# Kernel optimization log

Hardware: AMD Instinct MI355X
Metric: run time of the kernel (lower is better)

Reference implementation:

```python
import jax, jax.numpy as jnp
import numpy as np

M1 = 16
M2 = 16

def _spectral_conv(x, w1c, w2c):
    # x: [B,C,H,W] real; w*c: [C,C,M1,M2] complex
    B, C, H, W = x.shape
    xft = jnp.fft.rfft2(x)                      # [B,C,H,W//2+1]
    top = jnp.einsum('bixy,ioxy->boxy', xft[:, :, :M1, :M2], w1c)
    bot = jnp.einsum('bixy,ioxy->boxy', xft[:, :, -M1:, :M2], w2c)
    out_ft = jnp.zeros((B, w1c.shape[1], H, W // 2 + 1), dtype=xft.dtype)
    out_ft = out_ft.at[:, :, :M1, :M2].set(top)
    out_ft = out_ft.at[:, :, -M1:, :M2].set(bot)
    return jnp.fft.irfft2(out_ft, s=(H, W))

def _fourier_layer(x, w1c, w2c, cw, cb):
    x1 = _spectral_conv(x, w1c, w2c)
    x2 = jnp.einsum('bchw,oc->bohw', x, cw) + cb[None, :, None, None]  # 1x1 conv
    return jax.nn.gelu(x1 + x2, approximate=False)

def setup_inputs() -> dict:
    key = jax.random.key(0)
    ks = jax.random.split(key, 12)
    B, H, W, Tin, C, step = 8, 256, 256, 10, 32, 5
    scale = 1.0 / (C * C)
    return {
        'x': jax.random.normal(ks[0], (B, H, W, Tin), dtype=jnp.float32),
        'fc0_w': jax.random.normal(ks[1], (Tin + 2, C), dtype=jnp.float32) * 0.1,
        'fc0_b': jax.random.normal(ks[2], (C,), dtype=jnp.float32) * 0.1,
        'w1': jax.random.uniform(ks[3], (6, C, C, M1, M2, 2), dtype=jnp.float32) * scale,
        'w2': jax.random.uniform(ks[4], (6, C, C, M1, M2, 2), dtype=jnp.float32) * scale,
        'conv_w': jax.random.normal(ks[5], (6, C, C), dtype=jnp.float32) * 0.1,
        'conv_b': jax.random.normal(ks[6], (6, C), dtype=jnp.float32) * 0.1,
        'fc1_w': jax.random.normal(ks[7], (C, 128), dtype=jnp.float32) * 0.1,
        'fc1_b': jax.random.normal(ks[8], (128,), dtype=jnp.float32) * 0.1,
        'fc2_w': jax.random.normal(ks[9], (128, step), dtype=jnp.float32) * 0.1,
        'fc2_b': jax.random.normal(ks[10], (step,), dtype=jnp.float32) * 0.1,
    }

def reference(x, fc0_w, fc0_b, w1, w2, conv_w, conv_b, fc1_w, fc1_b, fc2_w, fc2_b):
    B, H, W, _ = x.shape
    gridx = jnp.broadcast_to(jnp.linspace(0.0, 1.0, H, dtype=x.dtype)[None, :, None, None], (B, H, W, 1))
    gridy = jnp.broadcast_to(jnp.linspace(0.0, 1.0, W, dtype=x.dtype)[None, None, :, None], (B, H, W, 1))
    h = jnp.concatenate([x, gridx, gridy], axis=-1)          # [B,H,W,T_in+2]
    h = jnp.einsum('bhwc,cd->bhwd', h, fc0_w) + fc0_b        # lift
    h = jnp.transpose(h, (0, 3, 1, 2))                        # [B,C,H,W]
    w1c = jax.lax.complex(w1[..., 0], w1[..., 1])
    w2c = jax.lax.complex(w2[..., 0], w2[..., 1])
    f = lambda z, i: _fourier_layer(z, w1c[i], w2c[i], conv_w[i], conv_b[i])
    h0 = f(h, 0)
    h = f(h, 1)
    h = f(h, 2) + h0
    h1 = f(h, 3)
    h = f(h, 4)
    h = f(h, 5) + h1
    h = jnp.transpose(h, (0, 2, 3, 1))                        # [B,H,W,C]
    h = jax.nn.gelu(jnp.einsum('bhwc,cd->bhwd', h, fc1_w) + fc1_b, approximate=False)
    return jnp.einsum('bhwc,cd->bhwd', h, fc2_w) + fc2_b      # [B,H,W,step]
```

## Files before the change

### kernel.cpp

```cpp
#include <hip/hip_runtime.h>
#include <math.h>

#define C_ 32
#define H_ 256
#define W_ 256
#define HW_ 65536
#define CHW_ 2097152
#define TWO_PI 6.28318530717958647692f

typedef __bf16 bf16x8 __attribute__((ext_vector_type(8)));
typedef float  f32x4  __attribute__((ext_vector_type(4)));

__device__ __forceinline__ bf16x8 as_bf16x8(uint4 u) {
    return __builtin_bit_cast(bf16x8, u);
}
__device__ __forceinline__ unsigned short bfbits(__bf16 h) {
    return __builtin_bit_cast(unsigned short, h);
}
__device__ __forceinline__ bf16x8 mk8(unsigned a, unsigned b, unsigned c, unsigned d) {
    return __builtin_bit_cast(bf16x8, make_uint4(a, b, c, d));
}
__device__ __forceinline__ unsigned rot16(unsigned v) { return (v >> 16) | (v << 16); }
__device__ __forceinline__ uint2 splitpack(float x, float y) {
    __bf16 xh = (__bf16)x, yh = (__bf16)y;
    float xl = x - (float)xh, yl = y - (float)yh;
    unsigned hi = (unsigned)bfbits(xh) | ((unsigned)bfbits(yh) << 16);
    unsigned lo = (unsigned)bfbits((__bf16)xl) | ((unsigned)bfbits((__bf16)yl) << 16);
    return make_uint2(hi, lo);
}

__device__ __forceinline__ float gelu_exact(float x) {
    return 0.5f * x * (1.0f + erff(x * 0.7071067811865475f));
}

__device__ __forceinline__ void build_tw(float2* tw, int tid) {
    float a = TWO_PI * (1.0f / 256.0f) * (float)tid;
    float s_, c_; sincosf(a, &s_, &c_);
    tw[tid] = make_float2(c_, s_);
}
__device__ __forceinline__ void build_twbf(uint2* twbf, int tid) {
    float a = TWO_PI * (1.0f / 256.0f) * (float)tid;
    float s_, c_; sincosf(a, &s_, &c_);
    twbf[tid] = splitpack(c_, s_);
}

__global__ void k_probe(float* __restrict__ out, float ws_kib) {
    if (threadIdx.x == 0 && blockIdx.x == 0) out[0] = ws_kib;
}

__global__ __launch_bounds__(256)
void k_lift(const float* __restrict__ xb, const float* __restrict__ fc0_w,
            const float* __restrict__ fc0_b, float* __restrict__ out) {
    __shared__ float wsh[12 * 32];
    __shared__ float bsh[32];
    int tid = threadIdx.x;
    for (int n = tid; n < 384; n += 256) wsh[n] = fc0_w[n];
    if (tid < 32) bsh[tid] = fc0_b[tid];
    __syncthreads();
    int p = blockIdx.x * 256 + tid;
    int w = p & 255;
    int h = (p >> 8) & 255;
    float in[12];
    const float* xp = xb + (size_t)p * 10;
    #pragma unroll
    for (int t = 0; t < 10; ++t) in[t] = xp[t];
    in[10] = (float)h * (1.0f / 255.0f);
    in[11] = (float)w * (1.0f / 255.0f);
    float* op = out + (p & 0xFFFF) + (size_t)(p >> 16) * CHW_;
    #pragma unroll
    for (int c = 0; c < 32; ++c) {
        float acc = bsh[c];
        #pragma unroll
        for (int t = 0; t < 12; ++t) acc += in[t] * wsh[t * 32 + c];
        op[(size_t)c * HW_] = acc;
    }
}

__global__ __launch_bounds__(256)
void k_dftw_mfma(const float* __restrict__ X, float* __restrict__ S, int nTiles) {
    __shared__ __align__(16) unsigned short twf[16384];
    int tid = threadIdx.x;
    for (int f = tid; f < 8192; f += 256) {
        int i  = f & 7;
        int c  = (f >> 3) & 15;
        int g  = (f >> 7) & 3;
        int nt = (f >> 9) & 1;
        int kk = f >> 10;
        int k  = kk * 32 + 8 * g + i;
        int j  = nt * 16 + c;
        int kx = j >> 1;
        int a  = (k * kx) & 255;
        float ang = (float)a * (TWO_PI / 256.0f);
        float s_, c_; sincosf(ang, &s_, &c_);
        float val = (j & 1) ? -s_ : c_;
        __bf16 hi = (__bf16)val;
        float  r  = val - (float)hi;
        __bf16 lo = (__bf16)r;
        twf[f]        = bfbits(hi);
        twf[8192 + f] = bfbits(lo);
    }
    __syncthreads();
    int wv   = tid >> 6;
    int lane = tid & 63;
    int kg   = lane >> 4;
    int cl   = lane & 15;
    const uint4* twp = (const uint4*)twf;
    for (int tile = blockIdx.x * 4 + wv; tile < nTiles; tile += gridDim.x * 4) {
        const float* xr = X + (size_t)(tile * 16 + cl) * 256 + 8 * kg;
        f32x4 acc0 = {0.f, 0.f, 0.f, 0.f};
        f32x4 acc1 = {0.f, 0.f, 0.f, 0.f};
        #pragma unroll
        for (int kk = 0; kk < 8; ++kk) {
            float4 a0 = *(const float4*)(xr + kk * 32);
            float4 a1 = *(const float4*)(xr + kk * 32 + 4);
            float xv[8] = {a0.x, a0.y, a0.z, a0.w, a1.x, a1.y, a1.z, a1.w};
            bf16x8 Ah, Al;
            #pragma unroll
            for (int i = 0; i < 8; ++i) {
                __bf16 h = (__bf16)xv[i];
                Ah[i] = h;
                Al[i] = (__bf16)(xv[i] - (float)h);
            }
            int base = kk * 128 + kg * 16 + cl;
            bf16x8 Bh0 = as_bf16x8(twp[base]);
            bf16x8 Bh1 = as_bf16x8(twp[base + 64]);
            bf16x8 Bl0 = as_bf16x8(twp[base + 1024]);
            bf16x8 Bl1 = as_bf16x8(twp[base + 1088]);
            acc0 = __builtin_amdgcn_mfma_f32_16x16x32_bf16(Al, Bl0, acc0, 0, 0, 0);
            acc0 = __builtin_amdgcn_mfma_f32_16x16x32_bf16(Ah, Bl0, acc0, 0, 0, 0);
            acc0 = __builtin_amdgcn_mfma_f32_16x16x32_bf16(Al, Bh0, acc0, 0, 0, 0);
            acc0 = __builtin_amdgcn_mfma_f32_16x16x32_bf16(Ah, Bh0, acc0, 0, 0, 0);
            acc1 = __builtin_amdgcn_mfma_f32_16x16x32_bf16(Al, Bl1, acc1, 0, 0, 0);
            acc1 = __builtin_amdgcn_mfma_f32_16x16x32_bf16(Ah, Bl1, acc1, 0, 0, 0);
            acc1 = __builtin_amdgcn_mfma_f32_16x16x32_bf16(Al, Bh1, acc1, 0, 0, 0);
            acc1 = __builtin_amdgcn_mfma_f32_16x16x32_bf16(Ah, Bh1, acc1, 0, 0, 0);
        }
        float* sp = S + (size_t)(tile * 16 + 4 * kg) * 32 + cl;
        #pragma unroll
        for (int q = 0; q < 4; ++q) {
            sp[q * 32]      = acc0[q];
            sp[q * 32 + 16] = acc1[q];
        }
    }
}

__global__ __launch_bounds__(256)
void k_dfth(const float* __restrict__ S, float* __restrict__ G) {
    __shared__ uint2 twbf[256];
    __shared__ uint2 slp[256][17];
    int tid = threadIdx.x;
    build_twbf(twbf, tid);
    const float2* sp = (const float2*)S + (size_t)blockIdx.x * 4096;
    #pragma unroll
    for (int i = 0; i < 16; ++i) {
        int n = i * 256 + tid;
        float2 v = sp[n];
        slp[n >> 4][n & 15] = splitpack(v.x, v.y);
    }
    __syncthreads();
    int wv = tid >> 6, lane = tid & 63, kg = lane >> 4, cl = lane & 15;
    int mt = wv >> 1, nt = wv & 1;
    int kyi_row = mt * 16 + cl;
    int ky = (kyi_row < 16) ? kyi_row : (kyi_row + 224);
    f32x4 acc = {0.f, 0.f, 0.f, 0.f};
    #pragma unroll 4
    for (int kk = 0; kk < 16; ++kk) {
        unsigned Ah[4], Al[4], Bh[4], Bl[4];
        #pragma unroll
        for (int j2 = 0; j2 < 4; ++j2) {
            int h = kk * 16 + kg * 4 + j2;
            uint2 t = twbf[(ky * h) & 255];
            Ah[j2] = t.x; Al[j2] = t.y;
            uint2 d = slp[h][cl];
            if (nt == 0) { Bh[j2] = d.x;                       Bl[j2] = d.y; }
            else         { Bh[j2] = rot16(d.x) ^ 0x80000000u;  Bl[j2] = rot16(d.y) ^ 0x80000000u; }
        }
        bf16x8 ah = mk8(Ah[0], Ah[1], Ah[2], Ah[3]);
        bf16x8 al = mk8(Al[0], Al[1], Al[2], Al[3]);
        bf16x8 bh = mk8(Bh[0], Bh[1], Bh[2], Bh[3]);
        bf16x8 bl = mk8(Bl[0], Bl[1], Bl[2], Bl[3]);
        acc = __builtin_amdgcn_mfma_f32_16x16x32_bf16(al, bl, acc, 0, 0, 0);
        acc = __builtin_amdgcn_mfma_f32_16x16x32_bf16(ah, bl, acc, 0, 0, 0);
        acc = __builtin_amdgcn_mfma_f32_16x16x32_bf16(al, bh, acc, 0, 0, 0);
        acc = __builtin_amdgcn_mfma_f32_16x16x32_bf16(ah, bh, acc, 0, 0, 0);
    }
    float* gf = G + (((size_t)blockIdx.x * 512 + (size_t)(mt * 16 + 4 * kg) * 16 + cl) * 2 + nt);
    #pragma unroll
    for (int q = 0; q < 4; ++q) gf[q * 32] = acc[q];
}

__global__ __launch_bounds__(256)
void k_mix(const float* __restrict__ G, const float* __restrict__ w1,
           const float* __restrict__ w2, float* __restrict__ G2) {
    int t = blockIdx.x * 256 + threadIdx.x;
    int kx  = t & 15;
    int kyi = (t >> 4) & 31;
    int o   = (t >> 9) & 31;
    int b   = t >> 14;
    const float* wp = (kyi < 16) ? w1 : w2;
    int kyj = kyi & 15;
    const float2* gp = (const float2*)G + (size_t)b * 16384 + (size_t)kyi * 16 + kx;
    float ar = 0.f, ai = 0.f;
    for (int i = 0; i < 32; ++i) {
        float2 g = gp[(size_t)i * 512];
        const float* wv = wp + ((((size_t)(i * 32 + o)) * 16 + kyj) * 16 + kx) * 2;
        ar += g.x * wv[0] - g.y * wv[1];
        ai += g.x * wv[1] + g.y * wv[0];
    }
    ((float2*)G2)[t] = make_float2(ar, ai);
}

__global__ __launch_bounds__(256)
void k_idfth(const float* __restrict__ G2, float* __restrict__ T) {
    __shared__ uint2 twbf[256];
    __shared__ uint2 gre[32][17];
    __shared__ uint2 gim[32][17];
    int tid = threadIdx.x;
    build_twbf(twbf, tid);
    const float2* gp = (const float2*)G2 + (size_t)blockIdx.x * 512;
    for (int n = tid; n < 512; n += 256) {
        float2 v = gp[n];
        gre[n >> 4][n & 15] = splitpack(v.x, -v.y);
        gim[n >> 4][n & 15] = splitpack(v.y,  v.x);
    }
    __syncthreads();
    int wv = tid >> 6, lane = tid & 63, kg = lane >> 4, cl = lane & 15;
    f32x4 accR[4] = {{0,0,0,0},{0,0,0,0},{0,0,0,0},{0,0,0,0}};
    f32x4 accI[4] = {{0,0,0,0},{0,0,0,0},{0,0,0,0},{0,0,0,0}};
    #pragma unroll
    for (int kk = 0; kk < 2; ++kk) {
        unsigned Brh[4], Brl[4], Bih[4], Bil[4];
        #pragma unroll
        for (int j2 = 0; j2 < 4; ++j2) {
            int kyi = kk * 16 + 4 * kg + j2;
            uint2 dr = gre[kyi][cl]; Brh[j2] = dr.x; Brl[j2] = dr.y;
            uint2 di = gim[kyi][cl]; Bih[j2] = di.x; Bil[j2] = di.y;
        }
        bf16x8 brh = mk8(Brh[0], Brh[1], Brh[2], Brh[3]);
        bf16x8 brl = mk8(Brl[0], Brl[1], Brl[2], Brl[3]);
        bf16x8 bih = mk8(Bih[0], Bih[1], Bih[2], Bih[3]);
        bf16x8 bil = mk8(Bil[0], Bil[1], Bil[2], Bil[3]);
        #pragma unroll
        for (int m = 0; m < 4; ++m) {
            int h = (wv * 4 + m) * 16 + cl;
            unsigned Ah[4], Al[4];
            #pragma unroll
            for (int j2 = 0; j2 < 4; ++j2) {
                int kyi = kk * 16 + 4 * kg + j2;
                int ky  = (kk == 0) ? kyi : (kyi + 224);
                uint2 t = twbf[(ky * h) & 255];
                Ah[j2] = t.x; Al[j2] = t.y;
            }
            bf16x8 ah = mk8(Ah[0], Ah[1], Ah[2], Ah[3]);
            bf16x8 al = mk8(Al[0], Al[1], Al[2], Al[3]);
            accR[m] = __builtin_amdgcn_mfma_f32_16x16x32_bf16(al, brl, accR[m], 0, 0, 0);
            accR[m] = __builtin_amdgcn_mfma_f32_16x16x32_bf16(ah, brl, accR[m], 0, 0, 0);
            accR[m] = __builtin_amdgcn_mfma_f32_16x16x32_bf16(al, brh, accR[m], 0, 0, 0);
            accR[m] = __builtin_amdgcn_mfma_f32_16x16x32_bf16(ah, brh, accR[m], 0, 0, 0);
            accI[m] = __builtin_amdgcn_mfma_f32_16x16x32_bf16(al, bil, accI[m], 0, 0, 0);
            accI[m] = __builtin_amdgcn_mfma_f32_16x16x32_bf16(ah, bil, accI[m], 0, 0, 0);
            accI[m] = __builtin_amdgcn_mfma_f32_16x16x32_bf16(al, bih, accI[m], 0, 0, 0);
            accI[m] = __builtin_amdgcn_mfma_f32_16x16x32_bf16(ah, bih, accI[m], 0, 0, 0);
        }
    }
    float sc = (cl == 0 ? 1.0f : 2.0f) * (1.0f / 65536.0f);
    float2* tp = (float2*)T;
    #pragma unroll
    for (int m = 0; m < 4; ++m) {
        #pragma unroll
        for (int q = 0; q < 4; ++q) {
            int h = (wv * 4 + m) * 16 + 4 * kg + q;
            tp[((size_t)blockIdx.x * 256 + h) * 16 + cl] =
                make_float2(accR[m][q] * sc, accI[m][q] * sc);
        }
    }
}

__global__ __launch_bounds__(256)
void k_invw_conv(const float* __restrict__ T, const float* X,
                 const float* __restrict__ cw, const float* __restrict__ cb,
                 const float* __restrict__ skip, float* Y) {
    __shared__ float2 tw[256];
    __shared__ float2 tsh[32][17];
    int tid = threadIdx.x;
    build_tw(tw, tid);
    int b  = blockIdx.x >> 8;
    int hh = blockIdx.x & 255;
    const float2* tp = (const float2*)T;
    for (int n = tid; n < 512; n += 256) {
        int o = n >> 4, kx = n & 15;
        tsh[o][kx] = tp[(((size_t)(b * 32 + o)) * 256 + hh) * 16 + kx];
    }
    __syncthreads();
    int wv = tid >> 6, lane = tid & 63;
    int kg = lane >> 4, cl = lane & 15;

    bf16x8 Ash[2], Asl[2];
    bf16x8 Ach[2], Acl2[2];
    #pragma unroll
    for (int mt = 0; mt < 2; ++mt) {
        int o = mt * 16 + cl;
        const float4* cwp = (const float4*)(cw + o * 32 + 8 * kg);
        float4 c0 = cwp[0], c1 = cwp[1];
        float cvv[8] = {c0.x, c0.y, c0.z, c0.w, c1.x, c1.y, c1.z, c1.w};
        #pragma unroll
        for (int j = 0; j < 8; ++j) {
            int k = 8 * kg + j;
            float2 tv = tsh[o][k >> 1];
            float v = (k & 1) ? -tv.y : tv.x;
            __bf16 hv = (__bf16)v;
            Ash[mt][j] = hv;
            Asl[mt][j] = (__bf16)(v - (float)hv);
            float cv = cvv[j];
            __bf16 hc = (__bf16)cv;
            Ach[mt][j]  = hc;
            Acl2[mt][j] = (__bf16)(cv - (float)hc);
        }
    }

    f32x4 acc[2][4];
    #pragma unroll
    for (int mt = 0; mt < 2; ++mt)
        #pragma unroll
        for (int nt = 0; nt < 4; ++nt)
            #pragma unroll
            for (int q = 0; q < 4; ++q)
                acc[mt][nt][q] = cb[mt * 16 + 4 * kg + q];

    const float* xb = X + (size_t)b * CHW_ + (size_t)hh * W_;
    #pragma unroll
    for (int nt = 0; nt < 4; ++nt) {
        int w = 64 * wv + 16 * nt + cl;
        bf16x8 Bth, Btl, Bxh, Bxl;
        #pragma unroll
        for (int j = 0; j < 8; ++j) {
            int k = 8 * kg + j;
            float2 cs = tw[((k >> 1) * w) & 255];
            float v = (k & 1) ? cs.y : cs.x;
            __bf16 hv = (__bf16)v;
            Bth[j] = hv;
            Btl[j] = (__bf16)(v - (float)hv);
            float xv = xb[(size_t)k * HW_ + w];
            __bf16 hx = (__bf16)xv;
            Bxh[j] = hx;
            Bxl[j] = (__bf16)(xv - (float)hx);
        }
        #pragma unroll
        for (int mt = 0; mt < 2; ++mt) {
            acc[mt][nt] = __builtin_amdgcn_mfma_f32_16x16x32_bf16(Asl[mt],  Btl, acc[mt][nt], 0, 0, 0);
            acc[mt][nt] = __builtin_amdgcn_mfma_f32_16x16x32_bf16(Ash[mt],  Btl, acc[mt][nt], 0, 0, 0);
            acc[mt][nt] = __builtin_amdgcn_mfma_f32_16x16x32_bf16(Asl[mt],  Bth, acc[mt][nt], 0, 0, 0);
            acc[mt][nt] = __builtin_amdgcn_mfma_f32_16x16x32_bf16(Ash[mt],  Bth, acc[mt][nt], 0, 0, 0);
            acc[mt][nt] = __builtin_amdgcn_mfma_f32_16x16x32_bf16(Acl2[mt], Bxl, acc[mt][nt], 0, 0, 0);
            acc[mt][nt] = __builtin_amdgcn_mfma_f32_16x16x32_bf16(Ach[mt],  Bxl, acc[mt][nt], 0, 0, 0);
            acc[mt][nt] = __builtin_amdgcn_mfma_f32_16x16x32_bf16(Acl2[mt], Bxh, acc[mt][nt], 0, 0, 0);
            acc[mt][nt] = __builtin_amdgcn_mfma_f32_16x16x32_bf16(Ach[mt],  Bxh, acc[mt][nt], 0, 0, 0);
        }
    }

    const bool hasSkip = (skip != nullptr);
    #pragma unroll
    for (int mt = 0; mt < 2; ++mt) {
        #pragma unroll
        for (int q = 0; q < 4; ++q) {
            int o = 16 * mt + 4 * kg + q;
            size_t rowbase = (size_t)b * CHW_ + (size_t)o * HW_ + (size_t)hh * W_;
            #pragma unroll
            for (int nt = 0; nt < 4; ++nt) {
                int w = 64 * wv + 16 * nt + cl;
                float g = gelu_exact(acc[mt][nt][q]);
                if (hasSkip) g += skip[rowbase + w];
                Y[rowbase + w] = g;
            }
        }
    }
}

__global__ __launch_bounds__(256)
void k_mlp(const float* __restrict__ X, const float* __restrict__ fc1_w,
           const float* __restrict__ fc1_b, const float* __restrict__ fc2_w,
           const float* __restrict__ fc2_b, float* __restrict__ outb) {
    int tid = threadIdx.x;
    int p0 = blockIdx.x * 512 + tid;
    int b  = p0 >> 16;
    int hw = p0 & 0xFFFF;
    const float* xp = X + (size_t)b * CHW_ + hw;
    float xv0[32], xv1[32];
    #pragma unroll
    for (int i = 0; i < 32; ++i) {
        xv0[i] = xp[(size_t)i * HW_];
        xv1[i] = xp[(size_t)i * HW_ + 256];
    }
    float o50[5] = {0.f, 0.f, 0.f, 0.f, 0.f};
    float o51[5] = {0.f, 0.f, 0.f, 0.f, 0.f};
    #pragma unroll 4
    for (int d = 0; d < 128; ++d) {
        float bd = fc1_b[d];
        float a0 = bd, a1 = bd;
        #pragma unroll
        for (int i = 0; i < 32; ++i) {
            float wv = fc1_w[i * 128 + d];
            a0 += xv0[i] * wv;
            a1 += xv1[i] * wv;
        }
        float g0 = gelu_exact(a0);
        float g1 = gelu_exact(a1);
        #pragma unroll
        for (int s = 0; s < 5; ++s) {
            float w2v = fc2_w[d * 5 + s];
            o50[s] += g0 * w2v;
            o51[s] += g1 * w2v;
        }
    }
    float* op0 = outb + (size_t)p0 * 5;
    #pragma unroll
    for (int s = 0; s < 5; ++s) op0[s] = o50[s] + fc2_b[s];
    float* op1 = outb + ((size_t)p0 + 256) * 5;
    #pragma unroll
    for (int s = 0; s < 5; ++s) op1[s] = o51[s] + fc2_b[s];
}

extern "C" void kernel_launch(void* const* d_in, const int* in_sizes, int n_in,
                              void* d_out, int out_size, void* d_ws, size_t ws_size,
                              hipStream_t stream) {
    const float* x      = (const float*)d_in[0];
    const float* fc0_w  = (const float*)d_in[1];
    const float* fc0_b  = (const float*)d_in[2];
    const float* w1     = (const float*)d_in[3];
    const float* w2     = (const float*)d_in[4];
    const float* conv_w = (const float*)d_in[5];
    const float* conv_b = (const float*)d_in[6];
    const float* fc1_w  = (const float*)d_in[7];
    const float* fc1_b  = (const float*)d_in[8];
    const float* fc2_w  = (const float*)d_in[9];
    const float* fc2_b  = (const float*)d_in[10];
    float* out = (float*)d_out;

    const size_t ACTb = 16777216;
    const size_t ACTi = 2097152;
    const size_t STb = 2097152, Gb = 262144;
    const size_t STi = 262144,  Gi = 32768;

    if (ws_size >= 2 * ACTb * sizeof(float)) {
        float* A0 = (float*)d_ws;
        float* A1 = A0 + ACTb;
        float* ST = out;
        float* G  = ST + STb;
        float* G2 = G + Gb;

        k_lift<<<2048, 256, 0, stream>>>(x, fc0_w, fc0_b, A0);
        auto layer = [&](int l, const float* Xin, float* Yout, const float* skip) {
            k_dftw_mfma<<<512, 256, 0, stream>>>(Xin, ST, 4096);
            k_dfth<<<256, 256, 0, stream>>>(ST, G);
            k_mix<<<512, 256, 0, stream>>>(G, w1 + (size_t)l * 524288,
                                           w2 + (size_t)l * 524288, G2);
            k_idfth<<<256, 256, 0, stream>>>(G2, ST);
            k_invw_conv<<<2048, 256, 0, stream>>>(ST, Xin, conv_w + (size_t)l * 1024,
                                                  conv_b + (size_t)l * 32, skip, Yout);
        };
        layer(0, A0, A1, nullptr);
        layer(1, A0, A0, nullptr);
        layer(2, A0, A0, A1);
        layer(3, A0, A1, nullptr);
        layer(4, A0, A0, nullptr);
        layer(5, A0, A0, A1);
        k_mlp<<<1024, 256, 0, stream>>>(A0, fc1_w, fc1_b, fc2_w, fc2_b, out);

    } else if (ws_size >= (3 * ACTi + STi + 2 * Gi) * sizeof(float)) {
        float* A0 = (float*)d_ws;
        float* A1 = A0 + ACTi;
        float* A2 = A1 + ACTi;
        float* ST = A2 + ACTi;
        float* G  = ST + STi;
        float* G2 = G + Gi;

        auto layer = [&](int l, const float* Xin, float* Yout, const float* skip) {
            k_dftw_mfma<<<64, 256, 0, stream>>>(Xin, ST, 512);
            k_dfth<<<32, 256, 0, stream>>>(ST, G);
            k_mix<<<64, 256, 0, stream>>>(G, w1 + (size_t)l * 524288,
                                          w2 + (size_t)l * 524288, G2);
            k_idfth<<<32, 256, 0, stream>>>(G2, ST);
            k_invw_conv<<<256, 256, 0, stream>>>(ST, Xin, conv_w + (size_t)l * 1024,
                                                 conv_b + (size_t)l * 32, skip, Yout);
        };
        for (int b = 0; b < 8; ++b) {
            k_lift<<<256, 256, 0, stream>>>(x + (size_t)b * HW_ * 10, fc0_w, fc0_b, A0);
            layer(0, A0, A2, nullptr);
            layer(1, A0, A1, nullptr);
            layer(2, A1, A0, A2);
            layer(3, A0, A2, nullptr);
            layer(4, A0, A1, nullptr);
            layer(5, A1, A0, A2);
            k_mlp<<<128, 256, 0, stream>>>(A0, fc1_w, fc1_b, fc2_w, fc2_b,
                                           out + (size_t)b * 327680);
        }
    } else {
        k_probe<<<1, 64, 0, stream>>>(out, (float)(ws_size >> 10));
    }
}
```

Before: 649.8 us.

## Run MLP head fc1 on MFMA with split-bf16 precision and shared-memory staging

Rewrites the final per-pixel MLP kernel so the 32x128 fc1 matmul runs on bf16 MFMA. Both operands are split into hi and lo bf16 parts and combined with four MFMAs to keep near-fp32 accuracy. Weights are packed into shared memory, the gelu outputs go to an LDS tile, and fc2 is done as a reduction across four lanes with shuffles. The grid becomes a grid-stride loop over 64-pixel chunks. The aim is to replace scalar FMA work and repeated global weight loads, at the cost of extra syncs and LDS traffic.

```diff
diff --git a/kernel.cpp b/kernel.cpp
--- a/kernel.cpp
+++ b/kernel.cpp
@@ -379,45 +379,80 @@
 __global__ __launch_bounds__(256)
 void k_mlp(const float* __restrict__ X, const float* __restrict__ fc1_w,
            const float* __restrict__ fc1_b, const float* __restrict__ fc2_w,
-           const float* __restrict__ fc2_b, float* __restrict__ outb) {
+           const float* __restrict__ fc2_b, float* __restrict__ outb, int nChunks) {
+    __shared__ uint2 w1p[2048];
+    __shared__ float bsh[128];
+    __shared__ float w2sh[640];
+    __shared__ float Gsh[64][133];
     int tid = threadIdx.x;
-    int p0 = blockIdx.x * 512 + tid;
-    int b  = p0 >> 16;
-    int hw = p0 & 0xFFFF;
-    const float* xp = X + (size_t)b * CHW_ + hw;
-    float xv0[32], xv1[32];
-    #pragma unroll
-    for (int i = 0; i < 32; ++i) {
-        xv0[i] = xp[(size_t)i * HW_];
-        xv1[i] = xp[(size_t)i * HW_ + 256];
-    }
-    float o50[5] = {0.f, 0.f, 0.f, 0.f, 0.f};
-    float o51[5] = {0.f, 0.f, 0.f, 0.f, 0.f};
-    #pragma unroll 4
-    for (int d = 0; d < 128; ++d) {
-        float bd = fc1_b[d];
-        float a0 = bd, a1 = bd;
-        #pragma unroll
-        for (int i = 0; i < 32; ++i) {
-            float wv = fc1_w[i * 128 + d];
-            a0 += xv0[i] * wv;
-            a1 += xv1[i] * wv;
-        }
-        float g0 = gelu_exact(a0);
-        float g1 = gelu_exact(a1);
-        #pragma unroll
-        for (int s = 0; s < 5; ++s) {
-            float w2v = fc2_w[d * 5 + s];
-            o50[s] += g0 * w2v;
-            o51[s] += g1 * w2v;
-        }
-    }
-    float* op0 = outb + (size_t)p0 * 5;
-    #pragma unroll
-    for (int s = 0; s < 5; ++s) op0[s] = o50[s] + fc2_b[s];
-    float* op1 = outb + ((size_t)p0 + 256) * 5;
-    #pragma unroll
-    for (int s = 0; s < 5; ++s) op1[s] = o51[s] + fc2_b[s];
+    for (int f = tid; f < 2048; f += 256) {
+        int j2 = f & 3, cl = (f >> 2) & 15, kg = (f >> 6) & 3, nt = f >> 8;
+        int d = nt * 16 + cl, k0 = 8 * kg + 2 * j2;
+        w1p[f] = splitpack(fc1_w[k0 * 128 + d], fc1_w[(k0 + 1) * 128 + d]);
+    }
+    if (tid < 128) bsh[tid] = fc1_b[tid];
+    for (int f = tid; f < 640; f += 256) w2sh[f] = fc2_w[f];
+    float b2[5];
+    #pragma unroll
+    for (int s = 0; s < 5; ++s) b2[s] = fc2_b[s];
+    int wv = tid >> 6, lane = tid & 63, kg = lane >> 4, cl = lane & 15;
+    int ploc2 = tid >> 2, dq = tid & 3;
+    __syncthreads();
+    for (int chunk = blockIdx.x; chunk < nChunks; chunk += gridDim.x) {
+        int P0 = chunk * 64;
+        int b  = P0 >> 16;
+        int hw0 = P0 & 0xFFFF;
+        {
+            const float* xp = X + (size_t)b * CHW_ + (size_t)(8 * kg) * HW_
+                            + (hw0 + wv * 16 + cl);
+            bf16x8 Ah, Al;
+            #pragma unroll
+            for (int j = 0; j < 8; ++j) {
+                float v = xp[(size_t)j * HW_];
+                __bf16 h = (__bf16)v;
+                Ah[j] = h;
+                Al[j] = (__bf16)(v - (float)h);
+            }
+            #pragma unroll
+            for (int nt = 0; nt < 8; ++nt) {
+                const uint2* wp = &w1p[((nt * 4 + kg) * 16 + cl) * 4];
+                uint2 q0 = wp[0], q1 = wp[1], q2 = wp[2], q3 = wp[3];
+                bf16x8 Bh = mk8(q0.x, q1.x, q2.x, q3.x);
+                bf16x8 Bl = mk8(q0.y, q1.y, q2.y, q3.y);
+                float bv = bsh[nt * 16 + cl];
+                f32x4 acc = {bv, bv, bv, bv};
+                acc = __builtin_amdgcn_mfma_f32_16x16x32_bf16(Al, Bl, acc, 0, 0, 0);
+                acc = __builtin_amdgcn_mfma_f32_16x16x32_bf16(Ah, Bl, acc, 0, 0, 0);
+                acc = __builtin_amdgcn_mfma_f32_16x16x32_bf16(Al, Bh, acc, 0, 0, 0);
+                acc = __builtin_amdgcn_mfma_f32_16x16x32_bf16(Ah, Bh, acc, 0, 0, 0);
+                #pragma unroll
+                for (int q = 0; q < 4; ++q)
+                    Gsh[wv * 16 + 4 * kg + q][nt * 16 + cl] = gelu_exact(acc[q]);
+            }
+        }
+        __syncthreads();
+        {
+            float a5[5] = {0.f, 0.f, 0.f, 0.f, 0.f};
+            #pragma unroll 8
+            for (int j = 0; j < 32; ++j) {
+                int d = dq + 4 * j;
+                float gv = Gsh[ploc2][d];
+                #pragma unroll
+                for (int s = 0; s < 5; ++s) a5[s] += gv * w2sh[d * 5 + s];
+            }
+            #pragma unroll
+            for (int s = 0; s < 5; ++s) {
+                a5[s] += __shfl_xor(a5[s], 1);
+                a5[s] += __shfl_xor(a5[s], 2);
+            }
+            if (dq == 0) {
+                float* op = outb + (size_t)(P0 + ploc2) * 5;
+                #pragma unroll
+                for (int s = 0; s < 5; ++s) op[s] = a5[s] + b2[s];
+            }
+        }
+        __syncthreads();
+    }
 }
 
 extern "C" void kernel_launch(void* const* d_in, const int* in_sizes, int n_in,
@@ -464,7 +499,7 @@
         layer(3, A0, A1, nullptr);
         layer(4, A0, A0, nullptr);
         layer(5, A0, A0, A1);
-        k_mlp<<<1024, 256, 0, stream>>>(A0, fc1_w, fc1_b, fc2_w, fc2_b, out);
+        k_mlp<<<2048, 256, 0, stream>>>(A0, fc1_w, fc1_b, fc2_w, fc2_b, out, 8192);
 
     } else if (ws_size >= (3 * ACTi + STi + 2 * Gi) * sizeof(float)) {
         float* A0 = (float*)d_ws;
@@ -491,8 +526,8 @@
             layer(3, A0, A2, nullptr);
             layer(4, A0, A1, nullptr);
             layer(5, A1, A0, A2);
-            k_mlp<<<128, 256, 0, stream>>>(A0, fc1_w, fc1_b, fc2_w, fc2_b,
-                                           out + (size_t)b * 327680);
+            k_mlp<<<1024, 256, 0, stream>>>(A0, fc1_w, fc1_b, fc2_w, fc2_b,
+                                            out + (size_t)b * 327680, 1024);
         }
     } else {
         k_probe<<<1, 64, 0, stream>>>(out, (float)(ws_size >> 10));
```

After: 606.7 us. 6.6% less time.
